# Optimization experiments

Measured on AMD Instinct MI355X. Metric: run time of the kernel, lower is better.

Reference implementation:

```python
import jax, jax.numpy as jnp
import numpy as np

MULTI_N_NUM = 2  # hardcoded in FCR.__init__
EPS = 1e-07


def setup_inputs() -> dict:
    key = jax.random.key(0)
    ka, kp, kn, ki = jax.random.split(key, 4)
    B, C, H, W = 32, 3, 256, 256
    a = jax.random.normal(ka, (B, C, H, W), dtype=jnp.float32)
    p = jax.random.normal(kp, (B, C, H, W), dtype=jnp.float32)
    n = jax.random.normal(kn, (B, C, H, W), dtype=jnp.float32)
    # sample_with_j(B, 2, i) -> [i, random j != i]; deterministic materialization
    offs = jax.random.randint(ki, (B, MULTI_N_NUM - 1), 1, B)  # in [1, B-1]
    base = jnp.arange(B, dtype=jnp.int64)
    other = (base[:, None] + offs.astype(jnp.int64)) % B
    neg_idx = jnp.concatenate([base[:, None], other], axis=1)  # [B, 2]
    return {"a": a, "p": p, "n": n, "neg_idx": neg_idx}


def reference(a, p, n, neg_idx):
    # FFT2 over the last two dims -> complex64
    a_fft = jnp.fft.fft2(a)
    p_fft = jnp.fft.fft2(p)
    n_fft = jnp.fft.fft2(n)
    # d_ap[i] = mean |a_fft[i] - p_fft[i]| over (C, H, W)
    d_ap = jnp.mean(jnp.abs(a_fft - p_fft), axis=(1, 2, 3))  # [B]
    # d_an[i, k] = mean |a_fft[i] - n_fft[neg_idx[i, k]]|
    n_gather = n_fft[neg_idx]                                  # [B, K, C, H, W]
    d_an = jnp.mean(jnp.abs(a_fft[:, None] - n_gather), axis=(2, 3, 4))  # [B, K]
    contrastive = jnp.sum(d_ap[:, None] / (d_an + EPS))
    return contrastive / (MULTI_N_NUM * a.shape[0])
```

## Files before the change

### kernel.cpp

```cpp
#include <hip/hip_runtime.h>
#include <hip/hip_fp16.h>
#include <math.h>

#define PIDX(e) ((e) + ((e) >> 4))

#define WAVE_SYNC()                          \
    do {                                     \
        __builtin_amdgcn_wave_barrier();     \
        asm volatile("" ::: "memory");       \
    } while (0)

__device__ __forceinline__ float2 cadd(float2 a, float2 b) { return {a.x + b.x, a.y + b.y}; }
__device__ __forceinline__ float2 csub(float2 a, float2 b) { return {a.x - b.x, a.y - b.y}; }
__device__ __forceinline__ float2 cmul(float2 a, float2 b) {
    return {a.x * b.x - a.y * b.y, a.x * b.y + a.y * b.x};
}

__device__ __forceinline__ void fft256_wave(float2* X, float2* Y, int t) {
    float2* sbuf = X;
    float2* dbuf = Y;
#pragma unroll
    for (int s = 0; s < 4; ++s) {
        const int sh = 2 * s;
        const int mm = 1 << sh;
        const int ll = 64 >> sh;
        const int jj = t >> sh;
        const int kk = t & (mm - 1);
        float2 c0 = sbuf[PIDX(kk + mm * jj)];
        float2 c1 = sbuf[PIDX(kk + mm * (jj + ll))];
        float2 c2 = sbuf[PIDX(kk + mm * (jj + 2 * ll))];
        float2 c3 = sbuf[PIDX(kk + mm * (jj + 3 * ll))];
        float2 sa = cadd(c0, c2);
        float2 sb = csub(c0, c2);
        float2 sc = cadd(c1, c3);
        float2 sd = {c1.y - c3.y, c3.x - c1.x};
        float2 d0 = cadd(sa, sc);
        float2 d1 = cadd(sb, sd);
        float2 d2 = csub(sa, sc);
        float2 d3 = csub(sb, sd);
        const float ang = -0.024543692606170259f * (float)(jj << sh);
        float sy, cx;
        __sincosf(ang, &sy, &cx);
        float2 w1 = {cx, sy};
        float2 w2 = cmul(w1, w1);
        float2 w3 = cmul(w2, w1);
        const int ob = kk + 4 * mm * jj;
        dbuf[PIDX(ob)] = d0;
        dbuf[PIDX(ob + mm)] = cmul(w1, d1);
        dbuf[PIDX(ob + 2 * mm)] = cmul(w2, d2);
        dbuf[PIDX(ob + 3 * mm)] = cmul(w3, d3);
        WAVE_SYNC();
        float2* tmp = sbuf;
        sbuf = dbuf;
        dbuf = tmp;
    }
}

__device__ __forceinline__ void load4(const float* __restrict__ abase,
                                      const float* __restrict__ sbase, int r, int t, float4& a0,
                                      float4& a1, float4& s0, float4& s1) {
    a0 = *(const float4*)(abase + (r << 8) + (t << 2));
    a1 = *(const float4*)(abase + ((r + 1) << 8) + (t << 2));
    s0 = *(const float4*)(sbase + (r << 8) + (t << 2));
    s1 = *(const float4*)(sbase + ((r + 1) << 8) + (t << 2));
}

__global__ __launch_bounds__(256) void k_rowfft(const float* __restrict__ A,
                                                const float* __restrict__ P,
                                                const float* __restrict__ N,
                                                const int* __restrict__ negIdx,
                                                __half2* __restrict__ ws, int img0) {
    __shared__ float2 Xb[4][272];
    __shared__ float2 Yb[4][272];
    __shared__ __half2 outT[128 * 33];

    const int img = img0 + blockIdx.y;
    const int pair = img / 3;
    const int ch = img - pair * 3;
    int i, jn;
    const float* S;
    if (pair < 32) {
        i = pair;
        jn = pair;
        S = P;
    } else {
        const int t2 = pair - 32;
        i = t2 >> 1;
        jn = negIdx[(i << 1) + (t2 & 1)];
        S = N;
    }
    const float* abase = A + ((size_t)(i * 3 + ch) << 16);
    const float* sbase = S + ((size_t)(jn * 3 + ch) << 16);

    const int tid = threadIdx.x;
    const int w = tid >> 6;
    const int t = tid & 63;
    const int r0 = blockIdx.x * 32;

    float4 pa0, pa1, ps0, ps1;
    load4(abase, sbase, r0 + 2 * w, t, pa0, pa1, ps0, ps1);

    for (int it = 0; it < 4; ++it) {
        const int slot = 2 * (it * 4 + w);
        const float4 a0 = pa0, a1 = pa1, s0 = ps0, s1 = ps1;
        if (it < 3) load4(abase, sbase, r0 + 2 * ((it + 1) * 4 + w), t, pa0, pa1, ps0, ps1);
        const int e0 = t << 2;
        Xb[w][PIDX(e0 + 0)] = {a0.x - s0.x, a1.x - s1.x};
        Xb[w][PIDX(e0 + 1)] = {a0.y - s0.y, a1.y - s1.y};
        Xb[w][PIDX(e0 + 2)] = {a0.z - s0.z, a1.z - s1.z};
        Xb[w][PIDX(e0 + 3)] = {a0.w - s0.w, a1.w - s1.w};
        WAVE_SYNC();
        fft256_wave(Xb[w], Yb[w], t);
        {
            const float2 p = Xb[w][PIDX(t)];
            if (t == 0) {
                const float2 z128 = Xb[w][PIDX(128)];
                outT[0 * 33 + slot] = __floats2half2_rn(p.x, z128.x);
                outT[0 * 33 + slot + 1] = __floats2half2_rn(p.y, z128.y);
            } else {
                const float2 m = Xb[w][PIDX(256 - t)];
                outT[t * 33 + slot] = __floats2half2_rn(0.5f * (p.x + m.x), 0.5f * (p.y - m.y));
                outT[t * 33 + slot + 1] =
                    __floats2half2_rn(0.5f * (p.y + m.y), -0.5f * (p.x - m.x));
            }
        }
        {
            const int v = t + 64;
            const float2 p = Xb[w][PIDX(v)];
            const float2 m = Xb[w][PIDX(192 - t)];
            outT[v * 33 + slot] = __floats2half2_rn(0.5f * (p.x + m.x), 0.5f * (p.y - m.y));
            outT[v * 33 + slot + 1] = __floats2half2_rn(0.5f * (p.y + m.y), -0.5f * (p.x - m.x));
        }
        WAVE_SYNC();
    }

    __syncthreads();

    __half2* g = ws + (size_t)blockIdx.y * (128 * 256);
    for (int e = tid; e < 128 * 8; e += 256) {
        const int v = e >> 3, rl4 = (e & 7) << 2;
        float4 val;
        __half2* vp = (__half2*)&val;
#pragma unroll
        for (int k = 0; k < 4; ++k) vp[k] = outT[v * 33 + rl4 + k];
        *(float4*)(g + v * 256 + r0 + rl4) = val;
    }
}

__global__ __launch_bounds__(256) void k_colfft(const __half2* __restrict__ ws,
                                                float* __restrict__ partial, int img0) {
    __shared__ float2 Xb[4][272];
    __shared__ float2 Yb[4][272];
    __shared__ float wsum[4];
    const int tid = threadIdx.x;
    const int w = tid >> 6, t = tid & 63;
    const int vbase = blockIdx.x * 16 + w * 4;
    const __half2* gimg = ws + (size_t)blockIdx.y * (128 * 256);

    float acc = 0.f;
    float4 nraw = *(const float4*)(gimg + (size_t)vbase * 256 + 4 * t);
    for (int j = 0; j < 4; ++j) {
        const int v = vbase + j;
        const float4 raw = nraw;
        if (j < 3) nraw = *(const float4*)(gimg + (size_t)(v + 1) * 256 + 4 * t);
        const __half2* hp = (const __half2*)&raw;
#pragma unroll
        for (int k = 0; k < 4; ++k) {
            const float2 z = __half22float2(hp[k]);
            Xb[w][PIDX(4 * t + k)] = z;
        }
        WAVE_SYNC();
        fft256_wave(Xb[w], Yb[w], t);
        float ssum = 0.f;
        if (v == 0) {
#pragma unroll
            for (int q = 0; q < 4; ++q) {
                const int u = t + 64 * q;
                const float2 zu = Xb[w][PIDX(u)];
                const float2 zm = Xb[w][PIDX((256 - u) & 255)];
                const float ax = 0.5f * (zu.x + zm.x), ay = 0.5f * (zu.y - zm.y);
                const float bx = 0.5f * (zu.y + zm.y), by = -0.5f * (zu.x - zm.x);
                ssum += sqrtf(ax * ax + ay * ay) + sqrtf(bx * bx + by * by);
            }
        } else {
#pragma unroll
            for (int q = 0; q < 4; ++q) {
                const float2 z = Xb[w][PIDX(t + 64 * q)];
                ssum += 2.f * sqrtf(z.x * z.x + z.y * z.y);
            }
        }
        acc += ssum;
        WAVE_SYNC();
    }
#pragma unroll
    for (int off = 32; off; off >>= 1) acc += __shfl_down(acc, off);
    if (t == 0) wsum[w] = acc;
    __syncthreads();
    if (tid == 0) {
        const int img = img0 + blockIdx.y;
        partial[img * 8 + blockIdx.x] = wsum[0] + wsum[1] + wsum[2] + wsum[3];
    }
}

__global__ void k_final(const float* __restrict__ partial, float* __restrict__ out) {
    __shared__ float ps[96];
    const int t = threadIdx.x;
    if (t < 96) {
        float s = 0.f;
        const float* p = partial + t * 24;
        for (int e = 0; e < 24; ++e) s += p[e];
        ps[t] = s;
    }
    __syncthreads();
    if (t < 64) {
        const float inv = 1.f / 196608.f;
        const float dap = ps[t >> 1] * inv;
        const float dan = ps[32 + t] * inv + 1e-7f;
        float val = dap / dan;
#pragma unroll
        for (int off = 32; off; off >>= 1) val += __shfl_down(val, off);
        if (t == 0) out[0] = val * (1.f / 64.f);
    }
}

extern "C" void kernel_launch(void* const* d_in, const int* in_sizes, int n_in,
                              void* d_out, int out_size, void* d_ws, size_t ws_size,
                              hipStream_t stream) {
    const float* A = (const float*)d_in[0];
    const float* P = (const float*)d_in[1];
    const float* N = (const float*)d_in[2];
    const int* negIdx = (const int*)d_in[3];

    float* partial = (float*)d_ws;
    __half2* inter = (__half2*)((char*)d_ws + 40960);
    const size_t perImg = (size_t)128 * 256 * sizeof(__half2);
    size_t avail = ws_size > 40960 ? ws_size - 40960 : 0;
    int cap = (int)(avail / perImg);
    if (cap > 288) cap = 288;
    if (cap < 1) cap = 1;

    for (int img0 = 0; img0 < 288; img0 += cap) {
        const int nimg = (288 - img0 < cap) ? (288 - img0) : cap;
        dim3 g1(8, nimg);
        k_rowfft<<<g1, dim3(256), 0, stream>>>(A, P, N, negIdx, inter, img0);
        dim3 g2(8, nimg);
        k_colfft<<<g2, dim3(256), 0, stream>>>(inter, partial, img0);
    }
    k_final<<<1, 128, 0, stream>>>(partial, (float*)d_out);
}
```

Before: 50.76 us.

## Run first FFT stage in registers and do remaining stages in place in LDS

Global loads now fetch strided elements (t, t+64, t+128, t+192) per lane so the first radix-4 butterfly is computed straight from registers, skipping one LDS write/read round. Later stages read all four inputs into registers, sync, then write back in place, which removes the ping-pong Y buffer and halves FFT shared memory. In exchange, vectorized float4 global loads become scalar strided loads, and each stage gains an extra wave barrier.

```diff
diff --git a/kernel.cpp b/kernel.cpp
--- a/kernel.cpp
+++ b/kernel.cpp
@@ -16,20 +16,42 @@
     return {a.x * b.x - a.y * b.y, a.x * b.y + a.y * b.x};
 }
 
-__device__ __forceinline__ void fft256_wave(float2* X, float2* Y, int t) {
-    float2* sbuf = X;
-    float2* dbuf = Y;
-#pragma unroll
-    for (int s = 0; s < 4; ++s) {
+__device__ __forceinline__ void fft256_stage0_reg(float2 z0, float2 z1, float2 z2, float2 z3,
+                                                  float2* X, int t) {
+    float2 sa = cadd(z0, z2);
+    float2 sb = csub(z0, z2);
+    float2 sc = cadd(z1, z3);
+    float2 sd = {z1.y - z3.y, z3.x - z1.x};
+    float2 d0 = cadd(sa, sc);
+    float2 d1 = cadd(sb, sd);
+    float2 d2 = csub(sa, sc);
+    float2 d3 = csub(sb, sd);
+    const float ang = -0.024543692606170259f * (float)t;
+    float sy, cx;
+    __sincosf(ang, &sy, &cx);
+    float2 w1 = {cx, sy};
+    float2 w2 = cmul(w1, w1);
+    float2 w3 = cmul(w2, w1);
+    const int ob = t << 2;
+    X[PIDX(ob)] = d0;
+    X[PIDX(ob + 1)] = cmul(w1, d1);
+    X[PIDX(ob + 2)] = cmul(w2, d2);
+    X[PIDX(ob + 3)] = cmul(w3, d3);
+    WAVE_SYNC();
+}
+
+__device__ __forceinline__ void fft256_stages123(float2* X, int t) {
+#pragma unroll
+    for (int s = 1; s < 4; ++s) {
+        float2 c0 = X[PIDX(t)];
+        float2 c1 = X[PIDX(t + 64)];
+        float2 c2 = X[PIDX(t + 128)];
+        float2 c3 = X[PIDX(t + 192)];
+        WAVE_SYNC();
         const int sh = 2 * s;
         const int mm = 1 << sh;
-        const int ll = 64 >> sh;
         const int jj = t >> sh;
         const int kk = t & (mm - 1);
-        float2 c0 = sbuf[PIDX(kk + mm * jj)];
-        float2 c1 = sbuf[PIDX(kk + mm * (jj + ll))];
-        float2 c2 = sbuf[PIDX(kk + mm * (jj + 2 * ll))];
-        float2 c3 = sbuf[PIDX(kk + mm * (jj + 3 * ll))];
         float2 sa = cadd(c0, c2);
         float2 sb = csub(c0, c2);
         float2 sc = cadd(c1, c3);
@@ -45,24 +67,24 @@
         float2 w2 = cmul(w1, w1);
         float2 w3 = cmul(w2, w1);
         const int ob = kk + 4 * mm * jj;
-        dbuf[PIDX(ob)] = d0;
-        dbuf[PIDX(ob + mm)] = cmul(w1, d1);
-        dbuf[PIDX(ob + 2 * mm)] = cmul(w2, d2);
-        dbuf[PIDX(ob + 3 * mm)] = cmul(w3, d3);
-        WAVE_SYNC();
-        float2* tmp = sbuf;
-        sbuf = dbuf;
-        dbuf = tmp;
-    }
-}
-
-__device__ __forceinline__ void load4(const float* __restrict__ abase,
-                                      const float* __restrict__ sbase, int r, int t, float4& a0,
-                                      float4& a1, float4& s0, float4& s1) {
-    a0 = *(const float4*)(abase + (r << 8) + (t << 2));
-    a1 = *(const float4*)(abase + ((r + 1) << 8) + (t << 2));
-    s0 = *(const float4*)(sbase + (r << 8) + (t << 2));
-    s1 = *(const float4*)(sbase + ((r + 1) << 8) + (t << 2));
+        X[PIDX(ob)] = d0;
+        X[PIDX(ob + mm)] = cmul(w1, d1);
+        X[PIDX(ob + 2 * mm)] = cmul(w2, d2);
+        X[PIDX(ob + 3 * mm)] = cmul(w3, d3);
+        WAVE_SYNC();
+    }
+}
+
+__device__ __forceinline__ void load16(const float* __restrict__ abase,
+                                       const float* __restrict__ sbase, int r, int t, float* a0,
+                                       float* a1, float* s0, float* s1) {
+#pragma unroll
+    for (int q = 0; q < 4; ++q) {
+        a0[q] = abase[(r << 8) + t + (q << 6)];
+        a1[q] = abase[((r + 1) << 8) + t + (q << 6)];
+        s0[q] = sbase[(r << 8) + t + (q << 6)];
+        s1[q] = sbase[((r + 1) << 8) + t + (q << 6)];
+    }
 }
 
 __global__ __launch_bounds__(256) void k_rowfft(const float* __restrict__ A,
@@ -71,7 +93,6 @@
                                                 const int* __restrict__ negIdx,
                                                 __half2* __restrict__ ws, int img0) {
     __shared__ float2 Xb[4][272];
-    __shared__ float2 Yb[4][272];
     __shared__ __half2 outT[128 * 33];
 
     const int img = img0 + blockIdx.y;
@@ -97,20 +118,17 @@
     const int t = tid & 63;
     const int r0 = blockIdx.x * 32;
 
-    float4 pa0, pa1, ps0, ps1;
-    load4(abase, sbase, r0 + 2 * w, t, pa0, pa1, ps0, ps1);
+    float pa0[4], pa1[4], ps0[4], ps1[4];
+    load16(abase, sbase, r0 + 2 * w, t, pa0, pa1, ps0, ps1);
 
     for (int it = 0; it < 4; ++it) {
         const int slot = 2 * (it * 4 + w);
-        const float4 a0 = pa0, a1 = pa1, s0 = ps0, s1 = ps1;
-        if (it < 3) load4(abase, sbase, r0 + 2 * ((it + 1) * 4 + w), t, pa0, pa1, ps0, ps1);
-        const int e0 = t << 2;
-        Xb[w][PIDX(e0 + 0)] = {a0.x - s0.x, a1.x - s1.x};
-        Xb[w][PIDX(e0 + 1)] = {a0.y - s0.y, a1.y - s1.y};
-        Xb[w][PIDX(e0 + 2)] = {a0.z - s0.z, a1.z - s1.z};
-        Xb[w][PIDX(e0 + 3)] = {a0.w - s0.w, a1.w - s1.w};
-        WAVE_SYNC();
-        fft256_wave(Xb[w], Yb[w], t);
+        float2 z[4];
+#pragma unroll
+        for (int q = 0; q < 4; ++q) z[q] = {pa0[q] - ps0[q], pa1[q] - ps1[q]};
+        if (it < 3) load16(abase, sbase, r0 + 2 * ((it + 1) * 4 + w), t, pa0, pa1, ps0, ps1);
+        fft256_stage0_reg(z[0], z[1], z[2], z[3], Xb[w], t);
+        fft256_stages123(Xb[w], t);
         {
             const float2 p = Xb[w][PIDX(t)];
             if (t == 0) {
@@ -150,7 +168,6 @@
 __global__ __launch_bounds__(256) void k_colfft(const __half2* __restrict__ ws,
                                                 float* __restrict__ partial, int img0) {
     __shared__ float2 Xb[4][272];
-    __shared__ float2 Yb[4][272];
     __shared__ float wsum[4];
     const int tid = threadIdx.x;
     const int w = tid >> 6, t = tid & 63;
@@ -158,19 +175,20 @@
     const __half2* gimg = ws + (size_t)blockIdx.y * (128 * 256);
 
     float acc = 0.f;
-    float4 nraw = *(const float4*)(gimg + (size_t)vbase * 256 + 4 * t);
+    __half2 cur[4], nxt[4];
+#pragma unroll
+    for (int q = 0; q < 4; ++q) cur[q] = gimg[(size_t)vbase * 256 + t + (q << 6)];
     for (int j = 0; j < 4; ++j) {
         const int v = vbase + j;
-        const float4 raw = nraw;
-        if (j < 3) nraw = *(const float4*)(gimg + (size_t)(v + 1) * 256 + 4 * t);
-        const __half2* hp = (const __half2*)&raw;
-#pragma unroll
-        for (int k = 0; k < 4; ++k) {
-            const float2 z = __half22float2(hp[k]);
-            Xb[w][PIDX(4 * t + k)] = z;
-        }
-        WAVE_SYNC();
-        fft256_wave(Xb[w], Yb[w], t);
+        if (j < 3) {
+#pragma unroll
+            for (int q = 0; q < 4; ++q) nxt[q] = gimg[(size_t)(v + 1) * 256 + t + (q << 6)];
+        }
+        float2 z[4];
+#pragma unroll
+        for (int q = 0; q < 4; ++q) z[q] = __half22float2(cur[q]);
+        fft256_stage0_reg(z[0], z[1], z[2], z[3], Xb[w], t);
+        fft256_stages123(Xb[w], t);
         float ssum = 0.f;
         if (v == 0) {
 #pragma unroll
@@ -185,11 +203,13 @@
         } else {
 #pragma unroll
             for (int q = 0; q < 4; ++q) {
-                const float2 z = Xb[w][PIDX(t + 64 * q)];
-                ssum += 2.f * sqrtf(z.x * z.x + z.y * z.y);
+                const float2 zz = Xb[w][PIDX(t + 64 * q)];
+                ssum += 2.f * sqrtf(zz.x * zz.x + zz.y * zz.y);
             }
         }
         acc += ssum;
+#pragma unroll
+        for (int q = 0; q < 4; ++q) cur[q] = nxt[q];
         WAVE_SYNC();
     }
 #pragma unroll
```

After: 46.91 us. 1.08x faster.
